# Performance work log

Hardware: AMD Instinct MI355X
Metric: run time of the kernel (lower is better)

The kernel has to match this reference:

```python
import jax, jax.numpy as jnp
import numpy as np

L, B, C, H, K = 2048, 2, 1024, 16, 9
FF = 4 * C  # conv FFN hidden channels


def _layer_norm(x, w, b, eps=1e-5):
    mu = jnp.mean(x, axis=-1, keepdims=True)
    var = jnp.mean((x - mu) ** 2, axis=-1, keepdims=True)
    return (x - mu) * jax.lax.rsqrt(var + eps) * w + b


def setup_inputs() -> dict:
    key = jax.random.key(0)
    ks = jax.random.split(key, 8)
    s = 0.02  # init scale for weights
    return {
        "x": jax.random.normal(ks[0], (L, B, C), dtype=jnp.float32),
        "mask": jnp.zeros((B, L), dtype=bool),
        "in_proj_w": jax.random.normal(ks[1], (3 * C, C), dtype=jnp.float32) * s,
        "in_proj_b": jnp.zeros((3 * C,), dtype=jnp.float32),
        "out_proj_w": jax.random.normal(ks[2], (C, C), dtype=jnp.float32) * s,
        "out_proj_b": jnp.zeros((C,), dtype=jnp.float32),
        "conv1_w": jax.random.normal(ks[3], (FF, C, K), dtype=jnp.float32) * s,
        "conv1_b": jnp.zeros((FF,), dtype=jnp.float32),
        "conv2_w": jax.random.normal(ks[4], (C, FF, 1), dtype=jnp.float32) * s,
        "conv2_b": jnp.zeros((C,), dtype=jnp.float32),
        "norm1_w": jnp.ones((C,), dtype=jnp.float32),
        "norm1_b": jnp.zeros((C,), dtype=jnp.float32),
        "norm2_w": jnp.ones((C,), dtype=jnp.float32),
        "norm2_b": jnp.zeros((C,), dtype=jnp.float32),
    }


def reference(x, mask, in_proj_w, in_proj_b, out_proj_w, out_proj_b,
              conv1_w, conv1_b, conv2_w, conv2_b,
              norm1_w, norm1_b, norm2_w, norm2_b):
    hd = C // H
    # --- self-attention ---
    qkv = x @ in_proj_w.T + in_proj_b            # (L, B, 3C)
    q, k, v = jnp.split(qkv, 3, axis=-1)

    def heads(t):  # (L, B, C) -> (B, H, L, hd)
        return t.reshape(L, B, H, hd).transpose(1, 2, 0, 3)

    q, k, v = heads(q), heads(k), heads(v)
    scores = jnp.einsum('bhqd,bhkd->bhqk', q, k) / jnp.sqrt(jnp.float32(hd))
    scores = jnp.where(mask[:, None, None, :], -jnp.inf, scores)
    attn = jax.nn.softmax(scores, axis=-1)
    ao = jnp.einsum('bhqk,bhkd->bhqd', attn, v)  # (B, H, L, hd)
    ao = ao.transpose(2, 0, 1, 3).reshape(L, B, C)
    ao = ao @ out_proj_w.T + out_proj_b
    x1 = _layer_norm(x + ao, norm1_w, norm1_b)
    # --- conv feed-forward ---
    xc = x1.transpose(1, 2, 0)                   # (B, C, L)
    dn = ('NCH', 'OIH', 'NCH')
    h = jax.lax.conv_general_dilated(xc, conv1_w, (1,), [(K // 2, K // 2)],
                                     dimension_numbers=dn)
    h = jax.nn.relu(h + conv1_b[None, :, None])
    h = jax.lax.conv_general_dilated(h, conv2_w, (1,), [(0, 0)],
                                     dimension_numbers=dn)
    h = h + conv2_b[None, :, None]
    return _layer_norm(x1 + h.transpose(2, 0, 1), norm2_w, norm2_b)
```

## Files before the change

### kernel.cpp

```cpp
#include <hip/hip_runtime.h>
#include <cstdint>
#include <cstddef>

#define LSEQ 2048
#define NB   2
#define CCH  1024
#define NHD  16
#define HDD  64
#define FFC  4096
#define KW   9
#define MROWS 4096

typedef __bf16 bf16x8 __attribute__((ext_vector_type(8)));
typedef float  floatx4 __attribute__((ext_vector_type(4)));
typedef unsigned short ushort4v __attribute__((ext_vector_type(4)));

__device__ inline unsigned short f2bf(float f) {
  union { float f; unsigned u; } v; v.f = f;
  unsigned r = v.u + 0x7FFFu + ((v.u >> 16) & 1u);
  return (unsigned short)(r >> 16);
}

__device__ inline void gload_lds16(const unsigned short* g, unsigned short* l) {
  __builtin_amdgcn_global_load_lds(
      (__attribute__((address_space(1))) unsigned int*)(g),
      (__attribute__((address_space(3))) unsigned int*)(l), 16, 0, 0);
}

__global__ void f2bf4_kernel(const float* __restrict__ in, unsigned short* __restrict__ out, int n4) {
  int idx = blockIdx.x * 256 + threadIdx.x;
  if (idx >= n4) return;
  const floatx4 v = ((const floatx4*)in)[idx];
  unsigned long long pk = (unsigned long long)f2bf(v[0]) |
                          ((unsigned long long)f2bf(v[1]) << 16) |
                          ((unsigned long long)f2bf(v[2]) << 32) |
                          ((unsigned long long)f2bf(v[3]) << 48);
  ((unsigned long long*)out)[idx] = pk;
}

__global__ __launch_bounds__(256) void repack_w1_kernel(const float* __restrict__ in,
                                                        unsigned short* __restrict__ out) {
  __shared__ unsigned short t[9216];
  const int f = blockIdx.x, tid = threadIdx.x;
  const float* src = in + (size_t)f * 9216;
#pragma unroll
  for (int rnd = 0; rnd < 9; ++rnd) {
    const int p = (rnd * 256 + tid) * 4;
    const floatx4 v = *(const floatx4*)(src + p);
#pragma unroll
    for (int e = 0; e < 4; ++e) {
      const int idx = p + e;
      const int c = idx / 9, k = idx - c * 9;
      t[k * 1024 + c] = f2bf(v[e]);
    }
  }
  __syncthreads();
  unsigned short* dst = out + (size_t)f * 9216;
#pragma unroll
  for (int rnd = 0; rnd < 9; ++rnd) {
    const int j = (rnd * 256 + tid) * 4;
    *(ushort4v*)(dst + j) = *(const ushort4v*)&t[j];
  }
}

__global__ void zero_u16(unsigned short* p, int n) {
  int idx = blockIdx.x * 256 + threadIdx.x;
  if (idx < n) p[idx] = 0;
}

__global__ __launch_bounds__(256) void transpose_v_kernel(
    const unsigned short* __restrict__ vin, unsigned short* __restrict__ vout) {
  __shared__ unsigned short t[64][65];
  const int tid = threadIdx.x;
  const int l0 = blockIdx.x * 64, bh = blockIdx.y;
  const unsigned short* src = vin + ((size_t)bh * LSEQ + l0) * HDD;
  const int rr = tid >> 4, cc = (tid & 15) * 4;
#pragma unroll
  for (int rnd = 0; rnd < 4; ++rnd) {
    const int row = rnd * 16 + rr;
    const ushort4v v = *(const ushort4v*)(src + row * HDD + cc);
#pragma unroll
    for (int e = 0; e < 4; ++e) t[row][cc + e] = v[e];
  }
  __syncthreads();
  unsigned short* dst = vout + (size_t)bh * HDD * LSEQ + l0;
#pragma unroll
  for (int rnd = 0; rnd < 4; ++rnd) {
    const int drow = rnd * 16 + rr;
    ushort4v v;
#pragma unroll
    for (int e = 0; e < 4; ++e) v[e] = t[cc + e][drow];
    *(ushort4v*)(dst + (size_t)drow * LSEQ + cc) = v;
  }
}

template <int EPI, bool KDEC, int BN>
__global__ __launch_bounds__(256) void gemm_bt(
    const unsigned short* __restrict__ A, const unsigned short* __restrict__ Bm,
    const float* __restrict__ bias, int N, int Kstride, int Klen,
    float* __restrict__ outF, float* __restrict__ outF2,
    unsigned short* __restrict__ outB,
    unsigned short* __restrict__ qb, unsigned short* __restrict__ kb,
    unsigned short* __restrict__ vb) {
  constexpr int JN = BN / 32;
  __shared__ alignas(16) unsigned short lA[128 * 32];
  __shared__ alignas(16) unsigned short lB[BN * 32];
  const int tid = threadIdx.x;
  const int m0 = blockIdx.x * 128;
  const int n0 = blockIdx.y * BN;
  const int z = blockIdx.z;
  A += (size_t)z * Klen;
  Bm += (size_t)z * Klen;
  const int wave = tid >> 6, lane = tid & 63;
  const int wm = (wave >> 1) * 64, wn = (wave & 1) * (BN / 2);
  const int l16 = lane & 15, quad = lane >> 4;
  const int fsw = (quad ^ ((l16 >> 1) & 3)) << 3;

  size_t aoff[2], boff[BN / 64];
#pragma unroll
  for (int i = 0; i < 2; ++i) {
    const int cf = i * 256 + tid;
    const int row = cf >> 2, cs = cf & 3;
    const int col = ((cs ^ ((row >> 1) & 3)) << 3);
    aoff[i] = (KDEC ? (size_t)row * 1024 : (size_t)(m0 + row) * Kstride) + col;
  }
#pragma unroll
  for (int i = 0; i < BN / 64; ++i) {
    const int cf = i * 256 + tid;
    const int row = cf >> 2, cs = cf & 3;
    const int col = ((cs ^ ((row >> 1) & 3)) << 3);
    boff[i] = (size_t)(n0 + row) * Kstride + col;
  }

  floatx4 acc[4][JN];
#pragma unroll
  for (int i = 0; i < 4; ++i)
#pragma unroll
    for (int j = 0; j < JN; ++j) acc[i][j] = (floatx4){0.f, 0.f, 0.f, 0.f};

  auto kstep = [&](const unsigned short* Ab, const unsigned short* Bb) {
    __syncthreads();
#pragma unroll
    for (int i = 0; i < 2; ++i)
      gload_lds16(Ab + aoff[i], &lA[(i * 256 + tid) * 8]);
#pragma unroll
    for (int i = 0; i < BN / 64; ++i)
      gload_lds16(Bb + boff[i], &lB[(i * 256 + tid) * 8]);
    __syncthreads();
    bf16x8 af[4], bf[JN];
#pragma unroll
    for (int i = 0; i < 4; ++i)
      af[i] = *(const bf16x8*)&lA[(wm + i * 16 + l16) * 32 + fsw];
#pragma unroll
    for (int j = 0; j < JN; ++j)
      bf[j] = *(const bf16x8*)&lB[(wn + j * 16 + l16) * 32 + fsw];
#pragma unroll
    for (int i = 0; i < 4; ++i)
#pragma unroll
      for (int j = 0; j < JN; ++j)
        acc[i][j] = __builtin_amdgcn_mfma_f32_16x16x32_bf16(af[i], bf[j], acc[i][j], 0, 0, 0);
  };

  if (KDEC) {
    for (int seg = 0; seg < KW; ++seg) {
      const unsigned short* Ab = A + (size_t)(m0 + seg * NB) * 1024;
      const unsigned short* Bb = Bm + seg * 1024;
      for (int kk = 0; kk < 1024; kk += 32) kstep(Ab + kk, Bb + kk);
    }
  } else {
    for (int k0 = 0; k0 < Klen; k0 += 32) kstep(A + k0, Bm + k0);
  }

  float* outZ = (z == 0) ? outF : outF2;
#pragma unroll
  for (int i = 0; i < 4; ++i) {
#pragma unroll
    for (int j = 0; j < JN; ++j) {
      const int colg = n0 + wn + j * 16 + l16;
      const int rbase = m0 + wm + i * 16 + quad * 4;
      const float bv = bias ? bias[colg] : 0.f;
      float vv[4];
#pragma unroll
      for (int r = 0; r < 4; ++r) vv[r] = acc[i][j][r] + bv;
      if (EPI == 1) {
#pragma unroll
        for (int r = 0; r < 4; ++r) outZ[(size_t)(rbase + r) * N + colg] = vv[r];
      } else if (EPI == 2) {
#pragma unroll
        for (int r = 0; r < 4; ++r)
          outB[(size_t)(rbase + r) * N + colg] = f2bf(fmaxf(vv[r], 0.f));
      } else {
        const int seg = colg >> 10;
        const int c = colg & 1023, h = c >> 6, d = c & 63;
        unsigned short* dst = (seg == 0) ? qb : (seg == 1) ? kb : vb;
        const float scl = (seg == 0) ? 0.125f : 1.f;
#pragma unroll
        for (int r = 0; r < 4; ++r) {
          const int row = rbase + r, l = row >> 1, b = row & 1;
          dst[(((size_t)(b * NHD + h)) * LSEQ + l) * HDD + d] = f2bf(vv[r] * scl);
        }
      }
    }
  }
}

#define WL   "s_waitcnt lgkmcnt(0)"
#define WV8L "s_waitcnt vmcnt(8) lgkmcnt(0)"
#define WV4L "s_waitcnt vmcnt(4) lgkmcnt(0)"
#define WV0L "s_waitcnt vmcnt(0) lgkmcnt(0)"
#define NOSTAGE ((void)0)

#define PHASE(p, kh, STA, STB, WAITSTR) do {                                   \
    asm volatile("" ::: "memory");                                             \
    const unsigned short* Ar_ = &lA[((p) * 2 + (kh)) * 8192];                  \
    const unsigned short* Br_ = &lB[((p) * 2 + (kh)) * 8192];                  \
    bf16x8 bfc_[4], af0_[4], af1_[4];                                          \
    _Pragma("unroll")                                                          \
    for (int j_ = 0; j_ < 4; ++j_)                                             \
      bfc_[j_] = *(const bf16x8*)&Br_[(wn * 64 + j_ * 16 + l16) * 32 + fsw];   \
    _Pragma("unroll")                                                          \
    for (int i_ = 0; i_ < 4; ++i_)                                             \
      af0_[i_] = *(const bf16x8*)&Ar_[(wm * 128 + i_ * 16 + l16) * 32 + fsw];  \
    _Pragma("unroll")                                                          \
    for (int i_ = 0; i_ < 4; ++i_)                                             \
      af1_[i_] = *(const bf16x8*)&Ar_[(wm * 128 + 64 + i_ * 16 + l16) * 32 + fsw]; \
    STA;                                                                       \
    STB;                                                                       \
    __builtin_amdgcn_s_setprio(1);                                             \
    _Pragma("unroll")                                                          \
    for (int i_ = 0; i_ < 4; ++i_)                                             \
      _Pragma("unroll")                                                        \
      for (int j_ = 0; j_ < 4; ++j_)                                           \
        acc[i_][j_] = __builtin_amdgcn_mfma_f32_16x16x32_bf16(                 \
            af0_[i_], bfc_[j_], acc[i_][j_], 0, 0, 0);                         \
    _Pragma("unroll")                                                          \
    for (int i_ = 0; i_ < 4; ++i_)                                             \
      _Pragma("unroll")                                                        \
      for (int j_ = 0; j_ < 4; ++j_)                                           \
        acc[4 + i_][j_] = __builtin_amdgcn_mfma_f32_16x16x32_bf16(             \
            af1_[i_], bfc_[j_], acc[4 + i_][j_], 0, 0, 0);                     \
    __builtin_amdgcn_s_setprio(0);                                             \
    asm volatile(WAITSTR ::: "memory");                                        \
    __builtin_amdgcn_s_barrier();                                              \
  } while (0)

__global__ __launch_bounds__(512, 2) void gemm256_conv1(
    const unsigned short* __restrict__ A,
    const unsigned short* __restrict__ Bm,
    const float* __restrict__ bias,
    unsigned short* __restrict__ outB) {
  __shared__ alignas(16) unsigned short lA[4 * 8192];
  __shared__ alignas(16) unsigned short lB[4 * 8192];
  const int tid = threadIdx.x;
  const int m0 = blockIdx.x * 256, n0 = blockIdx.y * 256;
  const int wave = tid >> 6, lane = tid & 63;
  const int wm = wave >> 2, wn = wave & 3;
  const int l16 = lane & 15, quad = lane >> 4;
  const int fsw = (quad ^ ((l16 >> 1) & 3)) << 3;

  unsigned int aoff[2], boff[2];
#pragma unroll
  for (int i = 0; i < 2; ++i) {
    const int cf = i * 512 + tid;
    const int row = cf >> 2, cs = cf & 3;
    const int col = (cs ^ ((row >> 1) & 3)) << 3;
    aoff[i] = (unsigned)(m0 + row) * 1024u + (unsigned)col;
    boff[i] = (unsigned)(n0 + row) * 9216u + (unsigned)col;
  }

  floatx4 acc[8][4];
#pragma unroll
  for (int i = 0; i < 8; ++i)
#pragma unroll
    for (int j = 0; j < 4; ++j) acc[i][j] = (floatx4){0.f, 0.f, 0.f, 0.f};

  auto stA = [&](int t, int kh) {
    const int p = t & 1;
    const unsigned koff = (unsigned)(t >> 4) * 2048u + (unsigned)((t & 15) * 64 + kh * 32);
#pragma unroll
    for (int i = 0; i < 2; ++i)
      gload_lds16(A + aoff[i] + koff, &lA[(p * 2 + kh) * 8192 + (i * 512 + tid) * 8]);
  };
  auto stB = [&](int t, int kh) {
    const int p = t & 1;
    const unsigned koff = (unsigned)t * 64u + (unsigned)(kh * 32);
#pragma unroll
    for (int i = 0; i < 2; ++i)
      gload_lds16(Bm + boff[i] + koff, &lB[(p * 2 + kh) * 8192 + (i * 512 + tid) * 8]);
  };

  stA(0, 0); stB(0, 0); stA(0, 1); stB(0, 1); stA(1, 0); stB(1, 0);
  asm volatile("s_waitcnt vmcnt(8)" ::: "memory");
  __builtin_amdgcn_s_barrier();

  const int NIT = 72;
  for (int it = 0; it < NIT - 1; ++it) {
    const int T = it * 2;
    PHASE(0, 0, stA(T + 1, 1), stB(T + 1, 1), WV8L);
    PHASE(0, 1, stA(T + 2, 0), stB(T + 2, 0), WV8L);
    PHASE(1, 0, stA(T + 2, 1), stB(T + 2, 1), WV8L);
    PHASE(1, 1, stA(T + 3, 0), stB(T + 3, 0), WV8L);
  }
  {
    PHASE(0, 0, stA(143, 1), stB(143, 1), WV8L);
    PHASE(0, 1, NOSTAGE, NOSTAGE, WV4L);
    PHASE(1, 0, NOSTAGE, NOSTAGE, WV0L);
    PHASE(1, 1, NOSTAGE, NOSTAGE, WL);
  }

#pragma unroll
  for (int ii = 0; ii < 8; ++ii) {
#pragma unroll
    for (int j = 0; j < 4; ++j) {
      const int colg = n0 + wn * 64 + j * 16 + l16;
      const int rbase = m0 + wm * 128 + ii * 16 + quad * 4;
      const float bv = bias[colg];
#pragma unroll
      for (int r = 0; r < 4; ++r)
        outB[(size_t)(rbase + r) * FFC + colg] = f2bf(fmaxf(acc[ii][j][r] + bv, 0.f));
    }
  }
}

__global__ __launch_bounds__(256) void attn_kernel(
    const unsigned short* __restrict__ qg, const unsigned short* __restrict__ kg,
    const unsigned short* __restrict__ vtg, unsigned short* __restrict__ ao) {
  __shared__ alignas(16) unsigned short lK[64 * 64];
  __shared__ alignas(16) unsigned short lV[64 * 64];
  __shared__ alignas(16) unsigned short lP[4][16 * 64];
  const int tid = threadIdx.x;
  const int wave = tid >> 6, lane = tid & 63;
  const int l16 = lane & 15, quad = lane >> 4;
  const int sw0 = ((quad ^ (l16 & 7)) << 3);
  const int sw1 = (((quad | 4) ^ (l16 & 7)) << 3);
  const int qt = blockIdx.x, h = blockIdx.y, b = blockIdx.z;
  const unsigned short* Q = qg + ((size_t)(b * NHD + h) * LSEQ) * HDD;
  const unsigned short* Kp = kg + ((size_t)(b * NHD + h) * LSEQ) * HDD;
  const unsigned short* Vt = vtg + ((size_t)(b * NHD + h) * HDD) * LSEQ;
  const int q0 = qt * 64 + wave * 16;

  const bf16x8 qa0 = *(const bf16x8*)&Q[(size_t)(q0 + l16) * HDD + quad * 8];
  const bf16x8 qa1 = *(const bf16x8*)&Q[(size_t)(q0 + l16) * HDD + 32 + quad * 8];

  float mr[4], lr[4];
  floatx4 o[4];
#pragma unroll
  for (int r = 0; r < 4; ++r) { mr[r] = -1e30f; lr[r] = 0.f; }
#pragma unroll
  for (int nb = 0; nb < 4; ++nb) o[nb] = (floatx4){0.f, 0.f, 0.f, 0.f};

  for (int kt = 0; kt < LSEQ; kt += 64) {
    __syncthreads();
#pragma unroll
    for (int i = 0; i < 2; ++i) {
      const int flat = i * 256 + tid;
      const int row = flat >> 3, cs = flat & 7;
      const int col = ((cs ^ (row & 7)) << 3);
      gload_lds16(&Kp[(size_t)(kt + row) * HDD + col], &lK[flat * 8]);
      gload_lds16(&Vt[(size_t)row * LSEQ + kt + col], &lV[flat * 8]);
    }
    __syncthreads();
    floatx4 s[4];
#pragma unroll
    for (int nb = 0; nb < 4; ++nb) {
      const bf16x8 kf0 = *(const bf16x8*)&lK[(nb * 16 + l16) * 64 + sw0];
      const bf16x8 kf1 = *(const bf16x8*)&lK[(nb * 16 + l16) * 64 + sw1];
      floatx4 t = (floatx4){0.f, 0.f, 0.f, 0.f};
      t = __builtin_amdgcn_mfma_f32_16x16x32_bf16(qa0, kf0, t, 0, 0, 0);
      t = __builtin_amdgcn_mfma_f32_16x16x32_bf16(qa1, kf1, t, 0, 0, 0);
      s[nb] = t;
    }
    float mnew[4], alpha[4];
#pragma unroll
    for (int r = 0; r < 4; ++r) {
      float mx = fmaxf(fmaxf(s[0][r], s[1][r]), fmaxf(s[2][r], s[3][r]));
      mx = fmaxf(mx, __shfl_xor(mx, 1));
      mx = fmaxf(mx, __shfl_xor(mx, 2));
      mx = fmaxf(mx, __shfl_xor(mx, 4));
      mx = fmaxf(mx, __shfl_xor(mx, 8));
      mnew[r] = fmaxf(mr[r], mx);
      alpha[r] = __expf(mr[r] - mnew[r]);
      mr[r] = mnew[r];
    }
#pragma unroll
    for (int nb = 0; nb < 4; ++nb)
#pragma unroll
      for (int r = 0; r < 4; ++r) s[nb][r] = __expf(s[nb][r] - mnew[r]);
#pragma unroll
    for (int r = 0; r < 4; ++r) {
      float sm = s[0][r] + s[1][r] + s[2][r] + s[3][r];
      sm += __shfl_xor(sm, 1);
      sm += __shfl_xor(sm, 2);
      sm += __shfl_xor(sm, 4);
      sm += __shfl_xor(sm, 8);
      lr[r] = lr[r] * alpha[r] + sm;
    }
#pragma unroll
    for (int nb = 0; nb < 4; ++nb)
#pragma unroll
      for (int r = 0; r < 4; ++r) {
        const int row = quad * 4 + r;
        const int q = nb * 2 + (l16 >> 3);
        lP[wave][row * 64 + ((q ^ (row & 7)) << 3) + (l16 & 7)] = f2bf(s[nb][r]);
        o[nb][r] *= alpha[r];
      }
    asm volatile("s_waitcnt lgkmcnt(0)" ::: "memory");
    const bf16x8 pa0 = *(const bf16x8*)&lP[wave][l16 * 64 + sw0];
    const bf16x8 pa1 = *(const bf16x8*)&lP[wave][l16 * 64 + sw1];
#pragma unroll
    for (int nb = 0; nb < 4; ++nb) {
      const bf16x8 vf0 = *(const bf16x8*)&lV[(nb * 16 + l16) * 64 + sw0];
      const bf16x8 vf1 = *(const bf16x8*)&lV[(nb * 16 + l16) * 64 + sw1];
      o[nb] = __builtin_amdgcn_mfma_f32_16x16x32_bf16(pa0, vf0, o[nb], 0, 0, 0);
      o[nb] = __builtin_amdgcn_mfma_f32_16x16x32_bf16(pa1, vf1, o[nb], 0, 0, 0);
    }
  }
#pragma unroll
  for (int nb = 0; nb < 4; ++nb)
#pragma unroll
    for (int r = 0; r < 4; ++r) {
      const float v = o[nb][r] / lr[r];
      const int lg = q0 + quad * 4 + r;
      ao[((size_t)lg * NB + b) * CCH + h * HDD + nb * 16 + l16] = f2bf(v);
    }
}

__global__ __launch_bounds__(256) void ln_kernel(
    const float* __restrict__ a, const float* __restrict__ c,
    const float* __restrict__ c2, const float* __restrict__ cbias,
    const float* __restrict__ w, const float* __restrict__ bias,
    float* __restrict__ outF, unsigned short* __restrict__ outB) {
  const int row = blockIdx.x;
  const int tid = threadIdx.x;
  const floatx4 va = *(const floatx4*)(a + (size_t)row * 1024 + tid * 4);
  const floatx4 vc = *(const floatx4*)(c + (size_t)row * 1024 + tid * 4);
  float v0 = va[0] + vc[0], v1 = va[1] + vc[1], v2 = va[2] + vc[2], v3 = va[3] + vc[3];
  if (c2) {
    const floatx4 v2c = *(const floatx4*)(c2 + (size_t)row * 1024 + tid * 4);
    v0 += v2c[0]; v1 += v2c[1]; v2 += v2c[2]; v3 += v2c[3];
  }
  if (cbias) {
    const floatx4 vb = *(const floatx4*)(cbias + tid * 4);
    v0 += vb[0]; v1 += vb[1]; v2 += vb[2]; v3 += vb[3];
  }
  float s = v0 + v1 + v2 + v3;
  float ss = v0 * v0 + v1 * v1 + v2 * v2 + v3 * v3;
#pragma unroll
  for (int off = 1; off < 64; off <<= 1) {
    s += __shfl_xor(s, off);
    ss += __shfl_xor(ss, off);
  }
  __shared__ float red[8];
  const int wave = tid >> 6, lane = tid & 63;
  if (lane == 0) { red[wave] = s; red[4 + wave] = ss; }
  __syncthreads();
  s = red[0] + red[1] + red[2] + red[3];
  ss = red[4] + red[5] + red[6] + red[7];
  const float mu = s * (1.f / 1024.f);
  const float var = ss * (1.f / 1024.f) - mu * mu;
  const float rs = rsqrtf(var + 1e-5f);
  const floatx4 wv = *(const floatx4*)(w + tid * 4);
  const floatx4 bv = *(const floatx4*)(bias + tid * 4);
  const float o0 = (v0 - mu) * rs * wv[0] + bv[0];
  const float o1 = (v1 - mu) * rs * wv[1] + bv[1];
  const float o2 = (v2 - mu) * rs * wv[2] + bv[2];
  const float o3 = (v3 - mu) * rs * wv[3] + bv[3];
  *(floatx4*)(outF + (size_t)row * 1024 + tid * 4) = (floatx4){o0, o1, o2, o3};
  if (outB) {
    unsigned long long pk = (unsigned long long)f2bf(o0) |
                            ((unsigned long long)f2bf(o1) << 16) |
                            ((unsigned long long)f2bf(o2) << 32) |
                            ((unsigned long long)f2bf(o3) << 48);
    *(unsigned long long*)(outB + (size_t)row * 1024 + tid * 4) = pk;
  }
}

extern "C" void kernel_launch(void* const* d_in, const int* in_sizes, int n_in,
                              void* d_out, int out_size, void* d_ws, size_t ws_size,
                              hipStream_t stream) {
  const float* x = (const float*)d_in[0];
  const float* wqkv = (const float*)d_in[2];
  const float* bqkv = (const float*)d_in[3];
  const float* wout = (const float*)d_in[4];
  const float* bout = (const float*)d_in[5];
  const float* w1 = (const float*)d_in[6];
  const float* b1 = (const float*)d_in[7];
  const float* w2 = (const float*)d_in[8];
  const float* b2 = (const float*)d_in[9];
  const float* n1w = (const float*)d_in[10];
  const float* n1b = (const float*)d_in[11];
  const float* n2w = (const float*)d_in[12];
  const float* n2b = (const float*)d_in[13];
  float* out = (float*)d_out;

  char* ws = (char*)d_ws;
  size_t off = 0;
  auto alloc = [&](size_t bytes) -> char* {
    char* p = ws + off;
    off += (bytes + 255) & ~(size_t)255;
    return p;
  };
  unsigned short* xb    = (unsigned short*)alloc((size_t)MROWS * 1024 * 2);
  unsigned short* wqkvb = (unsigned short*)alloc((size_t)3072 * 1024 * 2);
  unsigned short* woutb = (unsigned short*)alloc((size_t)1024 * 1024 * 2);
  unsigned short* w1p   = (unsigned short*)alloc((size_t)FFC * 9216 * 2);
  unsigned short* w2b   = (unsigned short*)alloc((size_t)1024 * FFC * 2);
  unsigned short* qbuf  = (unsigned short*)alloc((size_t)NB * NHD * LSEQ * HDD * 2);
  unsigned short* kbuf  = (unsigned short*)alloc((size_t)NB * NHD * LSEQ * HDD * 2);
  unsigned short* vtbuf = (unsigned short*)alloc((size_t)NB * NHD * LSEQ * HDD * 2);
  unsigned short* ao    = (unsigned short*)alloc((size_t)MROWS * 1024 * 2);
  float*          yz    = (float*)alloc((size_t)MROWS * 1024 * 4);
  float*          x1f   = (float*)alloc((size_t)MROWS * 1024 * 4);
  unsigned short* x1p   = (unsigned short*)alloc((size_t)(LSEQ + 8) * NB * 1024 * 2);
  unsigned short* hbuf  = (unsigned short*)alloc((size_t)MROWS * FFC * 2);
  if (off > ws_size) return;
  float*          yzB   = (float*)xb;
  unsigned short* vbuf  = hbuf;

  int n;
  n = MROWS * 1024 / 4; f2bf4_kernel<<<(n + 255) / 256, 256, 0, stream>>>(x, xb, n);
  n = 3072 * 1024 / 4;  f2bf4_kernel<<<(n + 255) / 256, 256, 0, stream>>>(wqkv, wqkvb, n);
  n = 1024 * 1024 / 4;  f2bf4_kernel<<<(n + 255) / 256, 256, 0, stream>>>(wout, woutb, n);
  n = 1024 * FFC / 4;   f2bf4_kernel<<<(n + 255) / 256, 256, 0, stream>>>(w2, w2b, n);
  repack_w1_kernel<<<FFC, 256, 0, stream>>>(w1, w1p);
  zero_u16<<<32, 256, 0, stream>>>(x1p, 8 * 1024);
  zero_u16<<<32, 256, 0, stream>>>(x1p + (size_t)(LSEQ + 4) * NB * 1024, 8 * 1024);

  gemm_bt<0, false, 128><<<dim3(32, 24), 256, 0, stream>>>(
      xb, wqkvb, bqkv, 3072, 1024, 1024, nullptr, nullptr, nullptr, qbuf, kbuf, vbuf);
  transpose_v_kernel<<<dim3(LSEQ / 64, NB * NHD), 256, 0, stream>>>(vbuf, vtbuf);
  attn_kernel<<<dim3(LSEQ / 64, NHD, NB), 256, 0, stream>>>(qbuf, kbuf, vtbuf, ao);
  gemm_bt<1, false, 64><<<dim3(32, 16), 256, 0, stream>>>(
      ao, woutb, bout, 1024, 1024, 1024, yz, nullptr, nullptr, nullptr, nullptr, nullptr);
  ln_kernel<<<MROWS, 256, 0, stream>>>(x, yz, nullptr, nullptr, n1w, n1b, x1f, x1p + 8 * 1024);
  gemm256_conv1<<<dim3(16, 16), 512, 0, stream>>>(x1p, w1p, b1, hbuf);
  gemm_bt<1, false, 64><<<dim3(32, 16, 2), 256, 0, stream>>>(
      hbuf, w2b, nullptr, 1024, FFC, 2048, yz, yzB, nullptr, nullptr, nullptr, nullptr);
  ln_kernel<<<MROWS, 256, 0, stream>>>(x1f, yz, yzB, b2, n2w, n2b, out, nullptr);
}
```

Before: 833.7 us.

## Software-pipeline LDS fragment reads across phases in conv1 GEMM

Restructures the conv1 GEMM main loop so the next phase's B fragments and first half of A fragments are read from LDS into a second register set partway through the current phase's MFMA sequence. Loads now alternate between two register sets. Wait counts change from vmcnt(8)+lgkmcnt(0) to vmcnt(4), and sched_barriers pin the ordering. The goal is to hide LDS read latency behind MFMA work, at the cost of about 64 extra VGPRs under a 512-thread, 2-block launch bound, which risks spills or lower occupancy. It also leans on tighter wait counts for correctness.

After: 828.0 us. Within noise of the previous version (-0.7%).

```diff
diff --git a/kernel.cpp b/kernel.cpp
--- a/kernel.cpp
+++ b/kernel.cpp
@@ -204,41 +204,49 @@
   }
 }
 
-#define WL   "s_waitcnt lgkmcnt(0)"
-#define WV8L "s_waitcnt vmcnt(8) lgkmcnt(0)"
-#define WV4L "s_waitcnt vmcnt(4) lgkmcnt(0)"
-#define WV0L "s_waitcnt vmcnt(0) lgkmcnt(0)"
+#define WV4 "s_waitcnt vmcnt(4)"
+#define WV0 "s_waitcnt vmcnt(0)"
+#define WNO "s_nop 0"
 #define NOSTAGE ((void)0)
 
-#define PHASE(p, kh, STA, STB, WAITSTR) do {                                   \
-    asm volatile("" ::: "memory");                                             \
-    const unsigned short* Ar_ = &lA[((p) * 2 + (kh)) * 8192];                  \
-    const unsigned short* Br_ = &lB[((p) * 2 + (kh)) * 8192];                  \
-    bf16x8 bfc_[4], af0_[4], af1_[4];                                          \
+#define RDPF(AA, BB, rg) do {                                                  \
+    const unsigned short* Pa_ = &lA[(rg) * 8192];                              \
+    const unsigned short* Pb_ = &lB[(rg) * 8192];                              \
     _Pragma("unroll")                                                          \
     for (int j_ = 0; j_ < 4; ++j_)                                             \
-      bfc_[j_] = *(const bf16x8*)&Br_[(wn * 64 + j_ * 16 + l16) * 32 + fsw];   \
+      BB[j_] = *(const bf16x8*)&Pb_[(wn * 64 + j_ * 16 + l16) * 32 + fsw];     \
     _Pragma("unroll")                                                          \
     for (int i_ = 0; i_ < 4; ++i_)                                             \
-      af0_[i_] = *(const bf16x8*)&Ar_[(wm * 128 + i_ * 16 + l16) * 32 + fsw];  \
+      AA[i_] = *(const bf16x8*)&Pa_[(wm * 128 + i_ * 16 + l16) * 32 + fsw];    \
+  } while (0)
+
+#define PHASE(rg, CA, CB, DO_PF, STA, STB, WAITSTR) do {                       \
+    asm volatile("" ::: "memory");                                             \
+    const unsigned short* Ar_ = &lA[(rg) * 8192];                              \
+    bf16x8 af1_[4];                                                            \
     _Pragma("unroll")                                                          \
     for (int i_ = 0; i_ < 4; ++i_)                                             \
       af1_[i_] = *(const bf16x8*)&Ar_[(wm * 128 + 64 + i_ * 16 + l16) * 32 + fsw]; \
     STA;                                                                       \
     STB;                                                                       \
+    __builtin_amdgcn_sched_barrier(0);                                         \
     __builtin_amdgcn_s_setprio(1);                                             \
     _Pragma("unroll")                                                          \
     for (int i_ = 0; i_ < 4; ++i_)                                             \
       _Pragma("unroll")                                                        \
       for (int j_ = 0; j_ < 4; ++j_)                                           \
         acc[i_][j_] = __builtin_amdgcn_mfma_f32_16x16x32_bf16(                 \
-            af0_[i_], bfc_[j_], acc[i_][j_], 0, 0, 0);                         \
+            CA[i_], CB[j_], acc[i_][j_], 0, 0, 0);                             \
+    __builtin_amdgcn_s_setprio(0);                                             \
+    DO_PF;                                                                     \
+    __builtin_amdgcn_sched_barrier(0);                                         \
+    __builtin_amdgcn_s_setprio(1);                                             \
     _Pragma("unroll")                                                          \
     for (int i_ = 0; i_ < 4; ++i_)                                             \
       _Pragma("unroll")                                                        \
       for (int j_ = 0; j_ < 4; ++j_)                                           \
         acc[4 + i_][j_] = __builtin_amdgcn_mfma_f32_16x16x32_bf16(             \
-            af1_[i_], bfc_[j_], acc[4 + i_][j_], 0, 0, 0);                     \
+            af1_[i_], CB[j_], acc[4 + i_][j_], 0, 0, 0);                       \
     __builtin_amdgcn_s_setprio(0);                                             \
     asm volatile(WAITSTR ::: "memory");                                        \
     __builtin_amdgcn_s_barrier();                                              \
@@ -274,6 +282,8 @@
 #pragma unroll
     for (int j = 0; j < 4; ++j) acc[i][j] = (floatx4){0.f, 0.f, 0.f, 0.f};
 
+  bf16x8 pa0[4], pb0[4], pa1[4], pb1[4];
+
   auto stA = [&](int t, int kh) {
     const int p = t & 1;
     const unsigned koff = (unsigned)(t >> 4) * 2048u + (unsigned)((t & 15) * 64 + kh * 32);
@@ -290,22 +300,23 @@
   };
 
   stA(0, 0); stB(0, 0); stA(0, 1); stB(0, 1); stA(1, 0); stB(1, 0);
-  asm volatile("s_waitcnt vmcnt(8)" ::: "memory");
+  asm volatile("s_waitcnt vmcnt(4)" ::: "memory");
   __builtin_amdgcn_s_barrier();
+  RDPF(pa0, pb0, 0);
 
   const int NIT = 72;
   for (int it = 0; it < NIT - 1; ++it) {
     const int T = it * 2;
-    PHASE(0, 0, stA(T + 1, 1), stB(T + 1, 1), WV8L);
-    PHASE(0, 1, stA(T + 2, 0), stB(T + 2, 0), WV8L);
-    PHASE(1, 0, stA(T + 2, 1), stB(T + 2, 1), WV8L);
-    PHASE(1, 1, stA(T + 3, 0), stB(T + 3, 0), WV8L);
+    PHASE(0, pa0, pb0, RDPF(pa1, pb1, 1), stA(T + 1, 1), stB(T + 1, 1), WV4);
+    PHASE(1, pa1, pb1, RDPF(pa0, pb0, 2), stA(T + 2, 0), stB(T + 2, 0), WV4);
+    PHASE(2, pa0, pb0, RDPF(pa1, pb1, 3), stA(T + 2, 1), stB(T + 2, 1), WV4);
+    PHASE(3, pa1, pb1, RDPF(pa0, pb0, 0), stA(T + 3, 0), stB(T + 3, 0), WV4);
   }
   {
-    PHASE(0, 0, stA(143, 1), stB(143, 1), WV8L);
-    PHASE(0, 1, NOSTAGE, NOSTAGE, WV4L);
-    PHASE(1, 0, NOSTAGE, NOSTAGE, WV0L);
-    PHASE(1, 1, NOSTAGE, NOSTAGE, WL);
+    PHASE(0, pa0, pb0, RDPF(pa1, pb1, 1), stA(143, 1), stB(143, 1), WV4);
+    PHASE(1, pa1, pb1, RDPF(pa0, pb0, 2), NOSTAGE, NOSTAGE, WV0);
+    PHASE(2, pa0, pb0, RDPF(pa1, pb1, 3), NOSTAGE, NOSTAGE, WV0);
+    PHASE(3, pa1, pb1, NOSTAGE, NOSTAGE, NOSTAGE, WNO);
   }
 
 #pragma unroll
```
